# Optimization experiments

Hardware: AMD Instinct MI355X
Metric: run time of the kernel (lower is better)

## Reference

```python
import jax, jax.numpy as jnp
import numpy as np

B, C, H, W = 16, 128, 56, 56
K = 3
F = K * K          # number of deformation filters = kernel taps
OUT = 512
STRIDE = 1


def setup_inputs() -> dict:
    key = jax.random.key(0)
    k1, k2, k3, k4 = jax.random.split(key, 4)
    x = jax.random.normal(k1, (B, C, H, W), jnp.float32)
    # Deform2d 1x1 offset conv: weight [2F, C], bias [2F] initialized to kernel tap offsets
    w_off = jax.random.normal(k2, (2 * F, C), jnp.float32) * 0.01
    half = K // 2
    xs = [float(dx) for dy in range(-half, K - half) for dx in range(-half, K - half)]
    ys = [float(dy) for dy in range(-half, K - half) for dx in range(-half, K - half)]
    b_off = jnp.array(xs + ys, jnp.float32)  # all x offsets first, then all y offsets
    # final 1x1 conv: [OUT, F*C]
    w_conv = jax.random.normal(k3, (OUT, F * C), jnp.float32) * (1.0 / np.sqrt(F * C))
    b_conv = jax.random.normal(k4, (OUT,), jnp.float32) * 0.01
    return {"x": x, "w_off": w_off, "b_off": b_off, "w_conv": w_conv, "b_conv": b_conv}


def _bilinear_sample(img, gx, gy):
    # img: [C,H,W]; gx, gy: [H,W] normalized coords in [-1,1]
    # torch grid_sample defaults: bilinear, zeros padding, align_corners=False
    C_, H_, W_ = img.shape
    ix = ((gx + 1.0) * W_ - 1.0) * 0.5
    iy = ((gy + 1.0) * H_ - 1.0) * 0.5
    x0 = jnp.floor(ix)
    y0 = jnp.floor(iy)
    wx1 = ix - x0
    wx0 = 1.0 - wx1
    wy1 = iy - y0
    wy0 = 1.0 - wy1

    def gather(yy, xx):
        valid = ((xx >= 0) & (xx < W_) & (yy >= 0) & (yy < H_)).astype(img.dtype)
        xi = jnp.clip(xx, 0, W_ - 1).astype(jnp.int32)
        yi = jnp.clip(yy, 0, H_ - 1).astype(jnp.int32)
        return img[:, yi, xi] * valid[None]  # [C,H,W]

    return (gather(y0, x0) * (wy0 * wx0)[None]
            + gather(y0, x0 + 1.0) * (wy0 * wx1)[None]
            + gather(y0 + 1.0, x0) * (wy1 * wx0)[None]
            + gather(y0 + 1.0, x0 + 1.0) * (wy1 * wx1)[None])


def reference(x, w_off, b_off, w_conv, b_conv):
    Bv, Cv, Hv, Wv = x.shape
    scale = 2.0 / max(Hv, Wv)
    # Deform2d: 1x1 conv -> per-pixel offsets, scaled to normalized grid units
    deform = (jnp.einsum('bchw,dc->bdhw', x, w_off) + b_off[None, :, None, None]) * scale
    # matches torch view(B*F, 2, H, W): consecutive channel pairs per filter
    deform = deform.reshape(Bv, F, 2, Hv, Wv)
    # identity grid from affine_grid (align_corners=False)
    base_x = (2.0 * jnp.arange(Wv, dtype=x.dtype) + 1.0) / Wv - 1.0
    base_y = (2.0 * jnp.arange(Hv, dtype=x.dtype) + 1.0) / Hv - 1.0
    # grid is detached in the torch code -> no gradient to the offset conv
    gx = jax.lax.stop_gradient(base_x[None, None, None, :] + deform[:, :, 0])  # [B,F,H,W]
    gy = jax.lax.stop_gradient(base_y[None, None, :, None] + deform[:, :, 1])  # [B,F,H,W]
    sample_f = jax.vmap(_bilinear_sample, in_axes=(None, 0, 0))   # over F filters (input shared)
    sample_bf = jax.vmap(sample_f, in_axes=(0, 0, 0))             # over batch
    sampled = sample_bf(x, gx, gy)                                 # [B,F,C,H,W]
    sampled = sampled.reshape(Bv, F * Cv, Hv, Wv)[:, :, ::STRIDE, ::STRIDE]
    # final 1x1 conv
    return jnp.einsum('bchw,oc->bohw', sampled, w_conv) + b_conv[None, :, None, None]
```

## Files before the change

kernel.cpp:

```cpp
#include <hip/hip_runtime.h>
#include <stdint.h>
#include <stddef.h>

#define BN 16
#define CN 128
#define HN 56
#define WN 56
#define HWN 3136
#define FN 9
#define DN 18
#define ON 512
#define KN 1152
#define MN 50176

typedef __bf16 bf16x8 __attribute__((ext_vector_type(8)));
typedef float f32x4 __attribute__((ext_vector_type(4)));

__device__ __forceinline__ unsigned short f2bf(float f) {
  unsigned int u = __builtin_bit_cast(unsigned int, f);
  u += 0x7fffu + ((u >> 16) & 1u);
  return (unsigned short)(u >> 16);
}

__device__ __forceinline__ void gload_lds16(const void* g, void* l) {
  __builtin_amdgcn_global_load_lds(
      (const __attribute__((address_space(1))) unsigned int*)g,
      (__attribute__((address_space(3))) unsigned int*)l, 16, 0, 0);
}

__global__ void k_transpose(const float* __restrict__ x, unsigned short* __restrict__ xt) {
  __shared__ float tile[32][33];
  const int b = blockIdx.z;
  const int hw0 = blockIdx.x * 32;
  const int c0 = blockIdx.y * 32;
  const int tx = threadIdx.x & 31;
  const int ty = threadIdx.x >> 5;
  const float* xb = x + (size_t)b * CN * HWN;
  unsigned short* xtb = xt + (size_t)b * HWN * CN;
#pragma unroll
  for (int r = 0; r < 4; ++r)
    tile[ty + r * 8][tx] = xb[(size_t)(c0 + ty + r * 8) * HWN + hw0 + tx];
  __syncthreads();
#pragma unroll
  for (int r = 0; r < 4; ++r)
    xtb[(size_t)(hw0 + ty + r * 8) * CN + c0 + tx] = f2bf(tile[tx][ty + r * 8]);
}

__global__ void k_wconv(const float4* __restrict__ w, ushort4* __restrict__ wb) {
  const int i = blockIdx.x * 256 + threadIdx.x;
  float4 v = w[i];
  ushort4 o;
  o.x = f2bf(v.x); o.y = f2bf(v.y); o.z = f2bf(v.z); o.w = f2bf(v.w);
  wb[i] = o;
}

__global__ void k_offsets(const unsigned short* __restrict__ xt, const float* __restrict__ w_off,
                          const float* __restrict__ b_off, float2* __restrict__ ixy) {
  const int m = blockIdx.x * 256 + threadIdx.x;
  const int b = m / HWN;
  const int hw = m - b * HWN;
  const int h = hw / WN;
  const int w = hw - h * WN;
  const unsigned short* xp = xt + (size_t)m * CN;
  float acc[DN];
#pragma unroll
  for (int d = 0; d < DN; ++d) acc[d] = b_off[d];
  for (int c = 0; c < CN; c += 8) {
    bf16x8 xv = *(const bf16x8*)(xp + c);
    float xf[8];
#pragma unroll
    for (int q = 0; q < 8; ++q) xf[q] = (float)xv[q];
#pragma unroll
    for (int d = 0; d < DN; ++d) {
      const float* wr = w_off + d * CN + c;
#pragma unroll
      for (int q = 0; q < 8; ++q) acc[d] += xf[q] * wr[q];
    }
  }
  const float scale = 2.0f / 56.0f;
  const float bx = (2.0f * w + 1.0f) / (float)WN - 1.0f;
  const float by = (2.0f * h + 1.0f) / (float)HN - 1.0f;
#pragma unroll
  for (int f = 0; f < FN; ++f) {
    float gx = bx + acc[2 * f] * scale;
    float gy = by + acc[2 * f + 1] * scale;
    float ixv = ((gx + 1.0f) * (float)WN - 1.0f) * 0.5f;
    float iyv = ((gy + 1.0f) * (float)HN - 1.0f) * 0.5f;
    ixy[(size_t)m * FN + f] = make_float2(ixv, iyv);
  }
}

__global__ void k_sample(const unsigned short* __restrict__ xt, const float2* __restrict__ ixy,
                         unsigned short* __restrict__ S) {
  const int g = blockIdx.x * 256 + threadIdx.x;
  const int cc = g & 7;
  const int mf = g >> 3;
  const int m = mf / FN;
  const int f = mf - m * FN;
  const int b = m / HWN;

  const float2 p = ixy[mf];
  const float ix = p.x, iy = p.y;
  const float x0f = floorf(ix), y0f = floorf(iy);
  const float wx1 = ix - x0f, wy1 = iy - y0f;
  const float wx0 = 1.0f - wx1, wy0 = 1.0f - wy1;
  const int x0 = (int)x0f, y0 = (int)y0f;
  const int x1 = x0 + 1, y1 = y0 + 1;
  const bool vx0 = (x0 >= 0) & (x0 < WN), vx1 = (x1 >= 0) & (x1 < WN);
  const bool vy0 = (y0 >= 0) & (y0 < HN), vy1 = (y1 >= 0) & (y1 < HN);
  const float w00 = wy0 * wx0 * ((vy0 & vx0) ? 1.0f : 0.0f);
  const float w01 = wy0 * wx1 * ((vy0 & vx1) ? 1.0f : 0.0f);
  const float w10 = wy1 * wx0 * ((vy1 & vx0) ? 1.0f : 0.0f);
  const float w11 = wy1 * wx1 * ((vy1 & vx1) ? 1.0f : 0.0f);
  const int x0c = min(max(x0, 0), WN - 1), x1c = min(max(x1, 0), WN - 1);
  const int y0c = min(max(y0, 0), HN - 1), y1c = min(max(y1, 0), HN - 1);

  const unsigned short* bp = xt + (size_t)b * HWN * CN + cc * 16;
  const bf16x8* p00 = (const bf16x8*)(bp + (size_t)(y0c * WN + x0c) * CN);
  const bf16x8* p01 = (const bf16x8*)(bp + (size_t)(y0c * WN + x1c) * CN);
  const bf16x8* p10 = (const bf16x8*)(bp + (size_t)(y1c * WN + x0c) * CN);
  const bf16x8* p11 = (const bf16x8*)(bp + (size_t)(y1c * WN + x1c) * CN);
  bf16x8 a0 = p00[0], a1 = p00[1];
  bf16x8 b0 = p01[0], b1 = p01[1];
  bf16x8 c0 = p10[0], c1 = p10[1];
  bf16x8 d0 = p11[0], d1 = p11[1];

  unsigned short ov[16];
#pragma unroll
  for (int q = 0; q < 8; ++q) {
    float lo = w00 * (float)a0[q] + w01 * (float)b0[q] + w10 * (float)c0[q] + w11 * (float)d0[q];
    float hi = w00 * (float)a1[q] + w01 * (float)b1[q] + w10 * (float)c1[q] + w11 * (float)d1[q];
    ov[q] = f2bf(lo);
    ov[q + 8] = f2bf(hi);
  }
  uint4* dst = (uint4*)(S + (size_t)m * KN + f * CN + cc * 16);
  dst[0] = *(const uint4*)(ov);
  dst[1] = *(const uint4*)(ov + 8);
}

__global__ __launch_bounds__(256) void k_gemm(const unsigned short* __restrict__ Wb,
                                              const unsigned short* __restrict__ S,
                                              const float* __restrict__ bias,
                                              float* __restrict__ out) {
  __shared__ __align__(16) char smem[32768];
  unsigned short* lw = (unsigned short*)smem;
  unsigned short* ls = (unsigned short*)(smem + 16384);
  const int tid = threadIdx.x;
  const int wave = tid >> 6;
  const int lane = tid & 63;
  const int quad = lane >> 4;
  const int r16 = lane & 15;
  const int o0 = blockIdx.x * 128;
  const int p0 = blockIdx.y * 128;
  const int wrow = wave >> 1;
  const int wcol = wave & 1;

  f32x4 acc[4][4];
#pragma unroll
  for (int i = 0; i < 4; ++i)
#pragma unroll
    for (int j = 0; j < 4; ++j) acc[i][j] = (f32x4){0.f, 0.f, 0.f, 0.f};

  const int row0 = tid >> 3;
  const int swc = (((tid & 7) ^ (row0 & 7))) * 8;
  const unsigned short* gw = Wb + (size_t)(o0 + row0) * KN + swc;
  const unsigned short* gs = S + (size_t)(p0 + row0) * KN + swc;
  unsigned short* lwd = lw + wave * 512;
  unsigned short* lsd = ls + wave * 512;

  const int rsw = r16 & 7;
  const int ch0 = (quad ^ rsw) * 8;
  const int ch1 = ((quad ^ rsw) ^ 4) * 8;
  const unsigned short* aw = lw + (wrow * 64 + r16) * 64;
  const unsigned short* bs = ls + (wcol * 64 + r16) * 64;

  for (int kt = 0; kt < KN / 64; ++kt) {
#pragma unroll
    for (int r = 0; r < 4; ++r) {
      gload_lds16(gw + (size_t)r * 32 * KN, lwd + r * 2048);
      gload_lds16(gs + (size_t)r * 32 * KN, lsd + r * 2048);
    }
    gw += 64; gs += 64;
    __syncthreads();
#pragma unroll
    for (int h = 0; h < 2; ++h) {
      const int ch = h ? ch1 : ch0;
      bf16x8 afr[4], bfr[4];
#pragma unroll
      for (int i = 0; i < 4; ++i) afr[i] = *(const bf16x8*)(aw + i * 16 * 64 + ch);
#pragma unroll
      for (int j = 0; j < 4; ++j) bfr[j] = *(const bf16x8*)(bs + j * 16 * 64 + ch);
#pragma unroll
      for (int i = 0; i < 4; ++i)
#pragma unroll
        for (int j = 0; j < 4; ++j)
          acc[i][j] = __builtin_amdgcn_mfma_f32_16x16x32_bf16(afr[i], bfr[j], acc[i][j], 0, 0, 0);
    }
    __syncthreads();
  }

  float* lout = (float*)smem;
  for (int half = 0; half < 2; ++half) {
    __syncthreads();
    if (wrow == half) {
#pragma unroll
      for (int i = 0; i < 4; ++i) {
        const int orow = i * 16 + quad * 4;
#pragma unroll
        for (int j = 0; j < 4; ++j) {
          const int col = wcol * 64 + j * 16 + r16;
          lout[(orow + 0) * 128 + col] = acc[i][j][0];
          lout[(orow + 1) * 128 + col] = acc[i][j][1];
          lout[(orow + 2) * 128 + col] = acc[i][j][2];
          lout[(orow + 3) * 128 + col] = acc[i][j][3];
        }
      }
    }
    __syncthreads();
#pragma unroll
    for (int t = 0; t < 8; ++t) {
      const int idx = t * 256 + tid;
      const int orow = idx >> 5;
      const int c4 = idx & 31;
      float4 v = ((const float4*)lout)[idx];
      const int o = o0 + half * 64 + orow;
      const float bv = bias[o];
      v.x += bv; v.y += bv; v.z += bv; v.w += bv;
      const int p = p0 + c4 * 4;
      const int bidx = p / HWN;
      const int hw = p - bidx * HWN;
      *(float4*)(out + (size_t)bidx * ON * HWN + (size_t)o * HWN + hw) = v;
    }
  }
}

extern "C" void kernel_launch(void* const* d_in, const int* in_sizes, int n_in,
                              void* d_out, int out_size, void* d_ws, size_t ws_size,
                              hipStream_t stream) {
  const float* x = (const float*)d_in[0];
  const float* w_off = (const float*)d_in[1];
  const float* b_off = (const float*)d_in[2];
  const float* w_conv = (const float*)d_in[3];
  const float* b_conv = (const float*)d_in[4];
  float* out = (float*)d_out;

  char* ws = (char*)d_ws;
  unsigned short* xt = (unsigned short*)(ws);
  unsigned short* S = (unsigned short*)(ws + 12845056);
  unsigned short* Wb = (unsigned short*)(ws + 128450560);
  float2* ixy = (float2*)(ws + 129630208);

  k_transpose<<<dim3(98, 4, 16), 256, 0, stream>>>(x, xt);
  k_wconv<<<dim3(576), 256, 0, stream>>>((const float4*)w_conv, (ushort4*)Wb);
  k_offsets<<<dim3(196), 256, 0, stream>>>(xt, w_off, b_off, ixy);
  k_sample<<<dim3(14112), 256, 0, stream>>>(xt, ixy, S);
  k_gemm<<<dim3(4, 392), 256, 0, stream>>>(Wb, S, b_conv, out);
}
```

Before: 269.7 us.

## Double-buffer GEMM LDS tiles, single-pass epilogue, and remap sample grid by filter

The GEMM now double-buffers its shared-memory tiles. The loads for the next K-tile are issued before the MFMAs on the current tile, and one barrier per iteration is removed. The epilogue writes the whole 128x128 accumulator tile to 64KB of LDS in one pass instead of two halves, which saves barriers. The sampling kernel uses a 2D grid with the filter index on blockIdx.y, so each block of threads shares one filter tap and the div/mod by 9 goes away. The cost is doubled LDS per block (64KB), which may lower occupancy.

```diff
diff --git a/kernel.cpp b/kernel.cpp
--- a/kernel.cpp
+++ b/kernel.cpp
@@ -92,14 +92,13 @@
 
 __global__ void k_sample(const unsigned short* __restrict__ xt, const float2* __restrict__ ixy,
                          unsigned short* __restrict__ S) {
-  const int g = blockIdx.x * 256 + threadIdx.x;
-  const int cc = g & 7;
-  const int mf = g >> 3;
-  const int m = mf / FN;
-  const int f = mf - m * FN;
+  const int tid = threadIdx.x;
+  const int cc = tid & 7;
+  const int m = blockIdx.x * 32 + (tid >> 3);
+  const int f = blockIdx.y;
   const int b = m / HWN;
 
-  const float2 p = ixy[mf];
+  const float2 p = ixy[(size_t)m * FN + f];
   const float ix = p.x, iy = p.y;
   const float x0f = floorf(ix), y0f = floorf(iy);
   const float wx1 = ix - x0f, wy1 = iy - y0f;
@@ -142,9 +141,9 @@
                                               const unsigned short* __restrict__ S,
                                               const float* __restrict__ bias,
                                               float* __restrict__ out) {
-  __shared__ __align__(16) char smem[32768];
-  unsigned short* lw = (unsigned short*)smem;
-  unsigned short* ls = (unsigned short*)(smem + 16384);
+  __shared__ __align__(16) char smem[65536];
+  unsigned short* lwB = (unsigned short*)smem;
+  unsigned short* lsB = (unsigned short*)(smem + 32768);
   const int tid = threadIdx.x;
   const int wave = tid >> 6;
   const int lane = tid & 63;
@@ -165,23 +164,35 @@
   const int swc = (((tid & 7) ^ (row0 & 7))) * 8;
   const unsigned short* gw = Wb + (size_t)(o0 + row0) * KN + swc;
   const unsigned short* gs = S + (size_t)(p0 + row0) * KN + swc;
-  unsigned short* lwd = lw + wave * 512;
-  unsigned short* lsd = ls + wave * 512;
+  const int ldst = wave * 512;
 
   const int rsw = r16 & 7;
   const int ch0 = (quad ^ rsw) * 8;
   const int ch1 = ((quad ^ rsw) ^ 4) * 8;
-  const unsigned short* aw = lw + (wrow * 64 + r16) * 64;
-  const unsigned short* bs = ls + (wcol * 64 + r16) * 64;
+  const int awo = (wrow * 64 + r16) * 64;
+  const int bso = (wcol * 64 + r16) * 64;
+
+#pragma unroll
+  for (int r = 0; r < 4; ++r) {
+    gload_lds16(gw + (size_t)r * 32 * KN, lwB + ldst + r * 2048);
+    gload_lds16(gs + (size_t)r * 32 * KN, lsB + ldst + r * 2048);
+  }
+  gw += 64; gs += 64;
+  __syncthreads();
 
   for (int kt = 0; kt < KN / 64; ++kt) {
-#pragma unroll
-    for (int r = 0; r < 4; ++r) {
-      gload_lds16(gw + (size_t)r * 32 * KN, lwd + r * 2048);
-      gload_lds16(gs + (size_t)r * 32 * KN, lsd + r * 2048);
-    }
-    gw += 64; gs += 64;
-    __syncthreads();
+    const int cur = (kt & 1) * 8192;
+    const int nxt = 8192 - cur;
+    if (kt < KN / 64 - 1) {
+#pragma unroll
+      for (int r = 0; r < 4; ++r) {
+        gload_lds16(gw + (size_t)r * 32 * KN, lwB + nxt + ldst + r * 2048);
+        gload_lds16(gs + (size_t)r * 32 * KN, lsB + nxt + ldst + r * 2048);
+      }
+      gw += 64; gs += 64;
+    }
+    const unsigned short* aw = lwB + cur + awo;
+    const unsigned short* bs = lsB + cur + bso;
 #pragma unroll
     for (int h = 0; h < 2; ++h) {
       const int ch = h ? ch1 : ch0;
@@ -200,37 +211,32 @@
   }
 
   float* lout = (float*)smem;
-  for (int half = 0; half < 2; ++half) {
-    __syncthreads();
-    if (wrow == half) {
-#pragma unroll
-      for (int i = 0; i < 4; ++i) {
-        const int orow = i * 16 + quad * 4;
-#pragma unroll
-        for (int j = 0; j < 4; ++j) {
-          const int col = wcol * 64 + j * 16 + r16;
-          lout[(orow + 0) * 128 + col] = acc[i][j][0];
-          lout[(orow + 1) * 128 + col] = acc[i][j][1];
-          lout[(orow + 2) * 128 + col] = acc[i][j][2];
-          lout[(orow + 3) * 128 + col] = acc[i][j][3];
-        }
-      }
-    }
-    __syncthreads();
-#pragma unroll
-    for (int t = 0; t < 8; ++t) {
-      const int idx = t * 256 + tid;
-      const int orow = idx >> 5;
-      const int c4 = idx & 31;
-      float4 v = ((const float4*)lout)[idx];
-      const int o = o0 + half * 64 + orow;
-      const float bv = bias[o];
-      v.x += bv; v.y += bv; v.z += bv; v.w += bv;
-      const int p = p0 + c4 * 4;
-      const int bidx = p / HWN;
-      const int hw = p - bidx * HWN;
-      *(float4*)(out + (size_t)bidx * ON * HWN + (size_t)o * HWN + hw) = v;
-    }
+#pragma unroll
+  for (int i = 0; i < 4; ++i) {
+    const int orow = wrow * 64 + i * 16 + quad * 4;
+#pragma unroll
+    for (int j = 0; j < 4; ++j) {
+      const int col = wcol * 64 + j * 16 + r16;
+      lout[(orow + 0) * 128 + col] = acc[i][j][0];
+      lout[(orow + 1) * 128 + col] = acc[i][j][1];
+      lout[(orow + 2) * 128 + col] = acc[i][j][2];
+      lout[(orow + 3) * 128 + col] = acc[i][j][3];
+    }
+  }
+  __syncthreads();
+#pragma unroll
+  for (int t = 0; t < 16; ++t) {
+    const int idx = t * 256 + tid;
+    const int orow = idx >> 5;
+    const int c4 = idx & 31;
+    float4 v = ((const float4*)lout)[idx];
+    const int o = o0 + orow;
+    const float bv = bias[o];
+    v.x += bv; v.y += bv; v.z += bv; v.w += bv;
+    const int p = p0 + c4 * 4;
+    const int bidx = p / HWN;
+    const int hw = p - bidx * HWN;
+    *(float4*)(out + (size_t)bidx * ON * HWN + (size_t)o * HWN + hw) = v;
   }
 }
 
@@ -253,6 +259,6 @@
   k_transpose<<<dim3(98, 4, 16), 256, 0, stream>>>(x, xt);
   k_wconv<<<dim3(576), 256, 0, stream>>>((const float4*)w_conv, (ushort4*)Wb);
   k_offsets<<<dim3(196), 256, 0, stream>>>(xt, w_off, b_off, ixy);
-  k_sample<<<dim3(14112), 256, 0, stream>>>(xt, ixy, S);
+  k_sample<<<dim3(1568, 9), 256, 0, stream>>>(xt, ixy, S);
   k_gemm<<<dim3(4, 392), 256, 0, stream>>>(Wb, S, b_conv, out);
 }
```

Result: slower. 305.2 us (+13.1%).
